# Kernel optimization log

Measured on AMD Instinct MI355X. Metric: run time of the kernel, lower is better.

## Reference

```python
import jax, jax.numpy as jnp
import numpy as np

H = 16        # num_attention_heads
KV = 4        # num_key_value_heads
HD = 128      # head_dim = hidden // H
N_REP = H // KV
ROPE_THETA = 10000.0


def _rope_cos_sin(T, dtype):
    inv_freq = 1.0 / (ROPE_THETA ** (jnp.arange(0, HD, 2, dtype=jnp.float32) / HD))
    pos = jnp.arange(T, dtype=jnp.float32)
    freqs = pos[:, None] * inv_freq[None, :]            # [T, HD/2]
    emb = jnp.concatenate([freqs, freqs], axis=-1)      # [T, HD]
    return jnp.cos(emb).astype(dtype), jnp.sin(emb).astype(dtype)


def _rotate_half(t):
    t1, t2 = jnp.split(t, 2, axis=-1)
    return jnp.concatenate([-t2, t1], axis=-1)


def setup_inputs() -> dict:
    key = jax.random.key(0)
    k1, k2, k3 = jax.random.split(key, 3)
    B, T, C = 2, 2048, 2048
    x = jax.random.normal(k1, (B, T, C), dtype=jnp.float32)
    attention_mask = jnp.ones((B, T), dtype=jnp.float32)
    w_qkv = jax.random.normal(k2, ((H + 2 * KV) * HD, C), dtype=jnp.float32) * 0.02
    w_proj = jax.random.normal(k3, (C, C), dtype=jnp.float32) * 0.02
    return {"x": x, "attention_mask": attention_mask, "w_qkv": w_qkv, "w_proj": w_proj}


def reference(x, attention_mask, w_qkv, w_proj):
    B, T, C = x.shape
    dtype = x.dtype
    neg = jnp.finfo(dtype).min

    # additive mask: causal (-big above diagonal) + padding ((1-mask)*min)
    i = jnp.arange(T)
    causal = jnp.where(i[None, :] <= i[:, None], 0.0, neg).astype(dtype)  # [T,T]
    add_mask = (1.0 - attention_mask)[:, None, None, :] * neg + causal[None, None]  # [B,1,T,T]

    # fused QKV projection
    qkv = jnp.einsum('btc,oc->bto', x, w_qkv)
    q = qkv[..., : H * HD].reshape(B, T, H, HD)
    k = qkv[..., H * HD : (H + KV) * HD].reshape(B, T, KV, HD)
    v = qkv[..., (H + KV) * HD :].reshape(B, T, KV, HD)

    # RoPE on q and k
    cos, sin = _rope_cos_sin(T, dtype)
    cos = cos[None, :, None, :]
    sin = sin[None, :, None, :]
    q = q * cos + _rotate_half(q) * sin
    k = k * cos + _rotate_half(k) * sin

    # GQA: repeat_interleave KV heads
    k = jnp.repeat(k, N_REP, axis=2)  # [B,T,H,HD]
    v = jnp.repeat(v, N_REP, axis=2)

    # [B,H,T,HD]
    q, k, v = (jnp.transpose(t, (0, 2, 1, 3)) for t in (q, k, v))

    scores = jnp.einsum('bhqd,bhkd->bhqk', q, k) * (1.0 / np.sqrt(HD))
    att = jax.nn.softmax(scores + add_mask, axis=-1)
    y = jnp.einsum('bhqk,bhkd->bhqd', att, v)
    y = jnp.transpose(y, (0, 2, 1, 3)).reshape(B, T, C)
    return jnp.einsum('btc,oc->bto', y, w_proj)
```

## Files before the change

kernel.cpp:

```cpp
#include <hip/hip_runtime.h>
#include <hip/hip_bf16.h>
#include <stdint.h>

typedef unsigned short u16;
typedef __attribute__((ext_vector_type(4))) float f32x4;
typedef __attribute__((ext_vector_type(8))) __bf16 bf16x8;
typedef __attribute__((ext_vector_type(8))) unsigned short u16x8;

#define NB 2
#define NT 2048
#define NC 2048
#define NH 16
#define NKV 4
#define HD 128
#define NQKV 3072
#define NQT 32
#define SCALE2 0.12751739f

__device__ __forceinline__ u16 f2bf(float f) {
  union { float f; uint32_t u; } c; c.f = f;
  uint32_t u = c.u + 0x7fffu + ((c.u >> 16) & 1u);
  return (u16)(u >> 16);
}
__device__ __forceinline__ float bf2f(u16 h) {
  union { uint32_t u; float f; } c; c.u = ((uint32_t)h) << 16;
  return c.f;
}
__device__ __forceinline__ uint32_t packbf2(float a, float b) {
  return (uint32_t)f2bf(a) | ((uint32_t)f2bf(b) << 16);
}

__device__ __forceinline__ void gload16(const void* g, void* lds) {
  __builtin_amdgcn_global_load_lds(
      (__attribute__((address_space(1))) void*)(uintptr_t)g,
      (__attribute__((address_space(3))) void*)(uint32_t)(uintptr_t)lds,
      16, 0, 0);
}

__global__ void cvt_bf16_kernel(const float* __restrict__ in, u16* __restrict__ out, int n4) {
  int i = blockIdx.x * blockDim.x + threadIdx.x;
  if (i >= n4) return;
  float4 v = ((const float4*)in)[i];
  uint32_t lo = (uint32_t)f2bf(v.x) | ((uint32_t)f2bf(v.y) << 16);
  uint32_t hi = (uint32_t)f2bf(v.z) | ((uint32_t)f2bf(v.w) << 16);
  ((uint2*)out)[i] = make_uint2(lo, hi);
}

__global__ void rope_tab_kernel(float* __restrict__ tab) {
  int idx = blockIdx.x * blockDim.x + threadIdx.x;
  int t = idx >> 6, i = idx & 63;
  float inv = expf(-(float)(2 * i) * (9.210340371976184f / 128.f));
  float f = (float)t * inv;
  tab[t * 128 + i] = cosf(f);
  tab[t * 128 + 64 + i] = sinf(f);
}

__global__ void rope_apply_kernel(const u16* __restrict__ qkv, const float* __restrict__ tab,
                                  u16* __restrict__ Q, u16* __restrict__ K) {
  int idx = blockIdx.x * blockDim.x + threadIdx.x;
  int i = idx & 63;
  int rest = idx >> 6;
  int hh = rest % 20;
  int bt = rest / 20;
  int t = bt & (NT - 1);
  int b = bt >> 11;
  const u16* src_row = qkv + (long)bt * NQKV;
  float c = tab[t * 128 + i], s = tab[t * 128 + 64 + i];
  if (hh < NH) {
    const u16* sp = src_row + hh * HD;
    float x0 = bf2f(sp[i]), x1 = bf2f(sp[i + 64]);
    u16* dp = Q + ((long)(b * NH + hh) * NT + t) * HD;
    dp[i] = f2bf((x0 * c - x1 * s) * SCALE2);
    dp[i + 64] = f2bf((x1 * c + x0 * s) * SCALE2);
  } else {
    int kh = hh - NH;
    const u16* sp = src_row + (NH + kh) * HD;
    float x0 = bf2f(sp[i]), x1 = bf2f(sp[i + 64]);
    u16* dp = K + ((long)(b * NKV + kh) * NT + t) * HD;
    dp[i] = f2bf(x0 * c - x1 * s);
    dp[i + 64] = f2bf(x1 * c + x0 * s);
  }
}

__global__ void vtrans_kernel(const u16* __restrict__ qkv, u16* __restrict__ Vt) {
  __shared__ u16 tile[64][72];
  const int t0 = (blockIdx.x >> 1) * 64;
  const int d0 = (blockIdx.x & 1) * 64;
  const int bkh = blockIdx.y;
  const int tid = threadIdx.x;
  const int tr = tid >> 2;
  const int tc = (tid & 3) * 16;
  const u16* src = qkv + ((long)((bkh >> 2) * NT) + t0 + tr) * NQKV +
                   (NH + NKV) * HD + (bkh & 3) * HD + d0 + tc;
  uint4 v0 = *(const uint4*)(src);
  uint4 v1 = *(const uint4*)(src + 8);
  *(uint4*)&tile[tr][tc] = v0;
  *(uint4*)&tile[tr][tc + 8] = v1;
  __syncthreads();
  const int dr = tid >> 2;
  const int tcc = (tid & 3) * 16;
  uint32_t pk[8];
#pragma unroll
  for (int e = 0; e < 8; ++e) {
    u16 a = tile[tcc + 2 * e][dr];
    u16 bq = tile[tcc + 2 * e + 1][dr];
    pk[e] = (uint32_t)a | ((uint32_t)bq << 16);
  }
  u16* dst = Vt + ((long)bkh * HD + d0 + dr) * NT + t0 + tcc;
  *(uint4*)(dst) = *(uint4*)&pk[0];
  *(uint4*)(dst + 8) = *(uint4*)&pk[4];
}

template <int OUT_BF16>
__global__ __launch_bounds__(256) void gemm_bt_kernel(const u16* __restrict__ A,
                                                      const u16* __restrict__ Bm,
                                                      void* __restrict__ Cm,
                                                      int M, int N, int K) {
  __shared__ __align__(16) u16 As[128 * 32];
  __shared__ __align__(16) u16 Bs[128 * 32];
  const int tid = threadIdx.x;
  const int lane = tid & 63;
  const int wid = tid >> 6;
  const long row0 = (long)blockIdx.y * 128;
  const long col0 = (long)blockIdx.x * 128;
  const int wr = (wid >> 1) * 64;
  const int wc = (wid & 1) * 64;
  const int g = lane >> 4;
  const int r = lane & 15;
  const int crow = lane >> 2;
  const int ccol = (lane & 3) * 8;
  const int c0 = wid * 2, c1 = wid * 2 + 1;

  f32x4 acc[4][4] = {};

  const u16* Abase0 = A + (row0 + c0 * 16 + crow) * (long)K + ccol;
  const u16* Abase1 = A + (row0 + c1 * 16 + crow) * (long)K + ccol;
  const u16* Bbase0 = Bm + (col0 + c0 * 16 + crow) * (long)K + ccol;
  const u16* Bbase1 = Bm + (col0 + c1 * 16 + crow) * (long)K + ccol;

  for (int k0 = 0; k0 < K; k0 += 32) {
    gload16(Abase0 + k0, &As[c0 * 512]);
    gload16(Abase1 + k0, &As[c1 * 512]);
    gload16(Bbase0 + k0, &Bs[c0 * 512]);
    gload16(Bbase1 + k0, &Bs[c1 * 512]);
    __syncthreads();
    bf16x8 af[4], bfr[4];
#pragma unroll
    for (int mi = 0; mi < 4; ++mi)
      af[mi] = *(const bf16x8*)&As[(wr + mi * 16 + r) * 32 + 8 * g];
#pragma unroll
    for (int ni = 0; ni < 4; ++ni)
      bfr[ni] = *(const bf16x8*)&Bs[(wc + ni * 16 + r) * 32 + 8 * g];
#pragma unroll
    for (int mi = 0; mi < 4; ++mi)
#pragma unroll
      for (int ni = 0; ni < 4; ++ni)
        acc[mi][ni] = __builtin_amdgcn_mfma_f32_16x16x32_bf16(af[mi], bfr[ni], acc[mi][ni], 0, 0, 0);
    __syncthreads();
  }
#pragma unroll
  for (int mi = 0; mi < 4; ++mi)
#pragma unroll
    for (int ni = 0; ni < 4; ++ni)
#pragma unroll
      for (int j = 0; j < 4; ++j) {
        long rr = row0 + wr + mi * 16 + g * 4 + j;
        long cc = col0 + wc + ni * 16 + r;
        float v = acc[mi][ni][j];
        if (OUT_BF16) ((u16*)Cm)[rr * N + cc] = f2bf(v);
        else          ((float*)Cm)[rr * N + cc] = v;
      }
}

__global__ __launch_bounds__(256) void attn_kernel(const u16* __restrict__ Qg,
                                                   const u16* __restrict__ Kg,
                                                   const u16* __restrict__ Vtg,
                                                   const float* __restrict__ amask,
                                                   u16* __restrict__ Y) {
  __shared__ __align__(16) u16 Ks[2][64 * 128];
  __shared__ __align__(16) u16 Vt[2][128 * 64];
  __shared__ __align__(16) u16 Ps[4][16 * 72];
  const int tid = threadIdx.x, lane = tid & 63, wid = tid >> 6;
  const int g = lane >> 4, r = lane & 15;
  const int h = blockIdx.y, b = blockIdx.z;
  const int kh = h >> 2;
  const int qta = blockIdx.x, qtb = NQT - 1 - qta;

  const u16* Kbh = Kg + (long)(b * NKV + kh) * NT * HD;
  const u16* Vtbh = Vtg + (long)(b * NKV + kh) * HD * NT;
  const u16* Qbh = Qg + (long)(b * NH + h) * NT * HD;
  const float* am_b = amask + b * NT;
  u16* Pw = &Ps[wid][0];

  const int total = qta + 1 + qtb + 1;

  const int krow_l = lane >> 4;
  const int kchunk = lane & 15;
  auto stageK = [&](u16* dst, int kv0) {
#pragma unroll
    for (int ii = 0; ii < 4; ++ii) {
      int kvl = (wid * 4 + ii) * 4 + krow_l;
      const u16* src = Kbh + (long)(kv0 + kvl) * HD + ((kchunk ^ (kvl & 7)) * 8);
      gload16(src, dst + (wid * 4 + ii) * 512);
    }
  };
  const int vrow_l = lane >> 3;
  const int vchunk = lane & 7;
  auto stageVt = [&](u16* dst, int kv0) {
#pragma unroll
    for (int ii = 0; ii < 4; ++ii) {
      int d = (wid * 4 + ii) * 8 + vrow_l;
      const u16* src = Vtbh + (long)d * NT + kv0 + ((vchunk ^ (d & 7)) * 8);
      gload16(src, dst + (wid * 4 + ii) * 512);
    }
  };

  bf16x8 qf[4];
  auto loadQ = [&](int q0) {
    const u16* Qrow = Qbh + (long)(q0 + wid * 16 + r) * HD;
#pragma unroll
    for (int kc = 0; kc < 4; ++kc)
      qf[kc] = *(const bf16x8*)(Qrow + kc * 32 + 8 * g);
  };

  stageK(Ks[0], 0);
  stageVt(Vt[0], 0);
  loadQ(qta * 64);
  __syncthreads();

  float m = -INFINITY;
  f32x4 lacc = {};
  f32x4 o[8] = {};
  int buf = 0;

  for (int i = 0; i < total; ++i) {
    const bool passA = (i <= qta);
    const int q0 = (passA ? qta : qtb) * 64;
    const int kt = passA ? i : i - qta - 1;
    const int kv0 = kt * 64;
    const bool diag = (i == qta) || (i == total - 1);
    const int qi = q0 + wid * 16 + r;

    if (i + 1 < total) {
      const int ktn = (i + 1 <= qta) ? i + 1 : i - qta;
      stageK(Ks[buf ^ 1], ktn * 64);
      stageVt(Vt[buf ^ 1], ktn * 64);
    }

    const u16* Ksb = Ks[buf];
    const u16* Vtb = Vt[buf];

    f32x4 s[4];
    __builtin_amdgcn_s_setprio(1);
#pragma unroll
    for (int cb = 0; cb < 4; ++cb) {
      f32x4 acc = {};
      int row = cb * 16 + r;
      int swz = (r & 7) << 4;
#pragma unroll
      for (int kc = 0; kc < 4; ++kc) {
        bf16x8 kf = *(const bf16x8*)((const char*)Ksb + ((row * 256 + (kc * 32 + 8 * g) * 2) ^ swz));
        acc = __builtin_amdgcn_mfma_f32_16x16x32_bf16(kf, qf[kc], acc, 0, 0, 0);
      }
      s[cb] = acc;
    }
    __builtin_amdgcn_s_setprio(0);

    if (diag) {
#pragma unroll
      for (int cb = 0; cb < 4; ++cb)
#pragma unroll
        for (int jj = 0; jj < 4; ++jj) {
          int kvi = kv0 + cb * 16 + 4 * g + jj;
          if (kvi > qi) s[cb][jj] = -INFINITY;
        }
    }

    float mxl = s[0][0];
#pragma unroll
    for (int cb = 0; cb < 4; ++cb)
#pragma unroll
      for (int jj = 0; jj < 4; ++jj) mxl = fmaxf(mxl, s[cb][jj]);
    if (!__all(mxl <= m + 8.f)) {
      float mx = mxl;
      mx = fmaxf(mx, __shfl_xor(mx, 16));
      mx = fmaxf(mx, __shfl_xor(mx, 32));
      float mnew = fmaxf(m, mx);
      float alpha = exp2f(m - mnew);
      m = mnew;
      lacc[0] *= alpha; lacc[1] *= alpha; lacc[2] *= alpha; lacc[3] *= alpha;
#pragma unroll
      for (int nb = 0; nb < 8; ++nb) {
        o[nb][0] *= alpha; o[nb][1] *= alpha; o[nb][2] *= alpha; o[nb][3] *= alpha;
      }
    }

    float4 amv[4];
#pragma unroll
    for (int cb = 0; cb < 4; ++cb)
      amv[cb] = *(const float4*)(am_b + kv0 + cb * 16 + 4 * g);

    float p[4][4];
#pragma unroll
    for (int cb = 0; cb < 4; ++cb)
#pragma unroll
      for (int jj = 0; jj < 4; ++jj) {
        float pv = exp2f(s[cb][jj] - m) * (&amv[cb].x)[jj];
        p[cb][jj] = pv;
        lacc[jj] += pv;
      }

#pragma unroll
    for (int cb = 0; cb < 4; ++cb) {
      union { __bf16 hh[4]; uint2 u; } pk;
      pk.hh[0] = (__bf16)p[cb][0]; pk.hh[1] = (__bf16)p[cb][1];
      pk.hh[2] = (__bf16)p[cb][2]; pk.hh[3] = (__bf16)p[cb][3];
      *(uint2*)((char*)Pw + 144 * r + 32 * cb + 8 * g) = pk.u;
    }
    asm volatile("s_waitcnt lgkmcnt(0)" ::: "memory");
    __builtin_amdgcn_sched_barrier(0);

    __builtin_amdgcn_s_setprio(1);
#pragma unroll
    for (int kc = 0; kc < 2; ++kc) {
      bf16x8 pb = *(const bf16x8*)((const char*)Pw + 144 * r + kc * 64 + 16 * g);
#pragma unroll
      for (int nb = 0; nb < 8; ++nb) {
        int d = nb * 16 + r;
        bf16x8 va = *(const bf16x8*)((const char*)Vtb +
            ((d * 128 + (kc * 32 + 8 * g) * 2) ^ ((d & 7) << 4)));
        o[nb] = __builtin_amdgcn_mfma_f32_16x16x32_bf16(va, pb, o[nb], 0, 0, 0);
      }
    }
    __builtin_amdgcn_s_setprio(0);

    if (diag) {
      float l = (lacc[0] + lacc[1]) + (lacc[2] + lacc[3]);
      l += __shfl_xor(l, 16);
      l += __shfl_xor(l, 32);
      float invl = 1.f / l;
      u16* Yrow = Y + ((long)b * NT + qi) * NC + h * HD;
#pragma unroll
      for (int nb = 0; nb < 8; ++nb)
        *(uint2*)(Yrow + nb * 16 + 4 * g) =
            make_uint2(packbf2(o[nb][0] * invl, o[nb][1] * invl),
                       packbf2(o[nb][2] * invl, o[nb][3] * invl));
      if (i == qta) {
        m = -INFINITY;
        lacc = f32x4{};
#pragma unroll
        for (int nb = 0; nb < 8; ++nb) o[nb] = f32x4{};
        loadQ(qtb * 64);
      }
    }

    __syncthreads();
    buf ^= 1;
  }
}

extern "C" void kernel_launch(void* const* d_in, const int* in_sizes, int n_in,
                              void* d_out, int out_size, void* d_ws, size_t ws_size,
                              hipStream_t stream) {
  const float* x = (const float*)d_in[0];
  const float* amask = (const float*)d_in[1];
  const float* w_qkv = (const float*)d_in[2];
  const float* w_proj = (const float*)d_in[3];

  const long MT = (long)NB * NT;
  char* ws = (char*)d_ws;
  size_t off = 0;
  auto carve = [&](size_t bytes) -> char* {
    char* p = ws + off;
    off += (bytes + 255) & ~(size_t)255;
    return p;
  };
  u16* xb   = (u16*)carve((size_t)MT * NC * 2);
  u16* wqb  = (u16*)carve((size_t)NQKV * NC * 2);
  u16* wpb  = (u16*)carve((size_t)NC * NC * 2);
  u16* qkvb = (u16*)carve((size_t)MT * NQKV * 2);
  float* tab = (float*)carve((size_t)NT * 128 * 4);

  u16* Qb = xb;
  u16* Kb = wqb;
  u16* Vtb = wqb + (size_t)NB * NKV * NT * HD;
  u16* Yb = qkvb;

  {
    int n4 = (int)(MT * NC / 4);
    cvt_bf16_kernel<<<dim3((n4 + 255) / 256), dim3(256), 0, stream>>>(x, xb, n4);
    n4 = (int)((long)NQKV * NC / 4);
    cvt_bf16_kernel<<<dim3((n4 + 255) / 256), dim3(256), 0, stream>>>(w_qkv, wqb, n4);
    n4 = (int)((long)NC * NC / 4);
    cvt_bf16_kernel<<<dim3((n4 + 255) / 256), dim3(256), 0, stream>>>(w_proj, wpb, n4);
  }
  rope_tab_kernel<<<dim3(NT * 64 / 256), dim3(256), 0, stream>>>(tab);
  gemm_bt_kernel<1><<<dim3(NQKV / 128, MT / 128), dim3(256), 0, stream>>>(xb, wqb, qkvb, (int)MT, NQKV, NC);
  rope_apply_kernel<<<dim3(NB * NT * 20 * 64 / 256), dim3(256), 0, stream>>>(qkvb, tab, Qb, Kb);
  vtrans_kernel<<<dim3(NT / 64 * 2, NB * NKV), dim3(256), 0, stream>>>(qkvb, Vtb);
  attn_kernel<<<dim3(NQT / 2, NH, NB), dim3(256), 0, stream>>>(Qb, Kb, Vtb, amask, Yb);
  gemm_bt_kernel<0><<<dim3(NC / 128, MT / 128), dim3(256), 0, stream>>>(Yb, wpb, d_out, (int)MT, NC, NC);
}
```

Baseline: 236.7 us.

## Rework attention to 32x32x16 MFMA with register-resident P and tiled V layout

The attention kernel moves from 16x16x32 to 32x32x16 MFMA. Each wave now handles 32 query rows, so the query tile per block grows to 128 and the grid shrinks to 8x16x2. Probabilities stay in registers as the B operand, which removes the per-wave LDS round trip and its waitcnt, and the V-transpose kernel writes a tiled, pair-interleaved layout that matches the new LDS swizzle. The tradeoff is fewer blocks (256 with launch bounds of one block per SM), higher register pressure, and a layout change that must stay consistent between the two kernels.

```diff
diff --git a/kernel.cpp b/kernel.cpp
--- a/kernel.cpp
+++ b/kernel.cpp
@@ -4,8 +4,8 @@
 
 typedef unsigned short u16;
 typedef __attribute__((ext_vector_type(4))) float f32x4;
+typedef __attribute__((ext_vector_type(16))) float f32x16;
 typedef __attribute__((ext_vector_type(8))) __bf16 bf16x8;
-typedef __attribute__((ext_vector_type(8))) unsigned short u16x8;
 
 #define NB 2
 #define NT 2048
@@ -14,7 +14,6 @@
 #define NKV 4
 #define HD 128
 #define NQKV 3072
-#define NQT 32
 #define SCALE2 0.12751739f
 
 __device__ __forceinline__ u16 f2bf(float f) {
@@ -106,7 +105,13 @@
     u16 bq = tile[tcc + 2 * e + 1][dr];
     pk[e] = (uint32_t)a | ((uint32_t)bq << 16);
   }
-  u16* dst = Vt + ((long)bkh * HD + d0 + dr) * NT + t0 + tcc;
+  uint32_t tmp;
+  tmp = pk[2]; pk[2] = pk[4]; pk[4] = tmp;
+  tmp = pk[3]; pk[3] = pk[5]; pk[5] = tmp;
+  const int d = d0 + dr;
+  const int t = t0 + tcc;
+  u16* dst = Vt + (long)bkh * HD * NT + (long)(d >> 1) * (2 * NT) +
+             (t >> 6) * 128 + (d & 1) * 64 + (t & 48);
   *(uint4*)(dst) = *(uint4*)&pk[0];
   *(uint4*)(dst + 8) = *(uint4*)&pk[4];
 }
@@ -172,185 +177,175 @@
       }
 }
 
-__global__ __launch_bounds__(256) void attn_kernel(const u16* __restrict__ Qg,
-                                                   const u16* __restrict__ Kg,
-                                                   const u16* __restrict__ Vtg,
-                                                   const float* __restrict__ amask,
-                                                   u16* __restrict__ Y) {
+__global__ __launch_bounds__(256, 1) void attn_kernel(const u16* __restrict__ Qg,
+                                                      const u16* __restrict__ Kg,
+                                                      const u16* __restrict__ Vtg,
+                                                      const float* __restrict__ amask,
+                                                      u16* __restrict__ Y) {
   __shared__ __align__(16) u16 Ks[2][64 * 128];
-  __shared__ __align__(16) u16 Vt[2][128 * 64];
-  __shared__ __align__(16) u16 Ps[4][16 * 72];
+  __shared__ __align__(16) u16 Vs[2][64 * 128];
   const int tid = threadIdx.x, lane = tid & 63, wid = tid >> 6;
-  const int g = lane >> 4, r = lane & 15;
+  const int ql = lane & 31, hi = lane >> 5;
   const int h = blockIdx.y, b = blockIdx.z;
   const int kh = h >> 2;
-  const int qta = blockIdx.x, qtb = NQT - 1 - qta;
+  const int qta = blockIdx.x, qtb = 15 - qta;
 
   const u16* Kbh = Kg + (long)(b * NKV + kh) * NT * HD;
   const u16* Vtbh = Vtg + (long)(b * NKV + kh) * HD * NT;
   const u16* Qbh = Qg + (long)(b * NH + h) * NT * HD;
   const float* am_b = amask + b * NT;
-  u16* Pw = &Ps[wid][0];
-
-  const int total = qta + 1 + qtb + 1;
-
-  const int krow_l = lane >> 4;
-  const int kchunk = lane & 15;
+
+  const int lenA = 2 * qta + 2;
+  const int total = lenA + 2 * qtb + 2;
+
+  const int srow = lane >> 4;
+  const int schunk = lane & 15;
   auto stageK = [&](u16* dst, int kv0) {
 #pragma unroll
     for (int ii = 0; ii < 4; ++ii) {
-      int kvl = (wid * 4 + ii) * 4 + krow_l;
-      const u16* src = Kbh + (long)(kv0 + kvl) * HD + ((kchunk ^ (kvl & 7)) * 8);
-      gload16(src, dst + (wid * 4 + ii) * 512);
+      int kvl = wid * 16 + ii * 4 + srow;
+      const u16* src = Kbh + (long)(kv0 + kvl) * HD + ((schunk ^ (kvl & 15)) * 8);
+      gload16(src, dst + (wid * 16 + ii * 4) * 128);
     }
   };
-  const int vrow_l = lane >> 3;
-  const int vchunk = lane & 7;
-  auto stageVt = [&](u16* dst, int kv0) {
+  auto stageV = [&](u16* dst, int kv0) {
+    const u16* vb = Vtbh + (kv0 >> 6) * 128;
 #pragma unroll
     for (int ii = 0; ii < 4; ++ii) {
-      int d = (wid * 4 + ii) * 8 + vrow_l;
-      const u16* src = Vtbh + (long)d * NT + kv0 + ((vchunk ^ (d & 7)) * 8);
-      gload16(src, dst + (wid * 4 + ii) * 512);
+      int R = wid * 16 + ii * 4 + srow;
+      const u16* src = vb + (long)R * (2 * NT) + ((schunk ^ (R & 15)) * 8);
+      gload16(src, dst + (wid * 16 + ii * 4) * 128);
     }
   };
 
-  bf16x8 qf[4];
+  bf16x8 qf[8];
   auto loadQ = [&](int q0) {
-    const u16* Qrow = Qbh + (long)(q0 + wid * 16 + r) * HD;
-#pragma unroll
-    for (int kc = 0; kc < 4; ++kc)
-      qf[kc] = *(const bf16x8*)(Qrow + kc * 32 + 8 * g);
+    const u16* Qrow = Qbh + (long)(q0 + wid * 32 + ql) * HD;
+#pragma unroll
+    for (int ks = 0; ks < 8; ++ks)
+      qf[ks] = *(const bf16x8*)(Qrow + ks * 16 + 8 * hi);
   };
 
   stageK(Ks[0], 0);
-  stageVt(Vt[0], 0);
-  loadQ(qta * 64);
+  stageV(Vs[0], 0);
+  loadQ(qta * 128);
   __syncthreads();
 
   float m = -INFINITY;
   f32x4 lacc = {};
-  f32x4 o[8] = {};
+  f32x16 o[4] = {};
   int buf = 0;
 
   for (int i = 0; i < total; ++i) {
-    const bool passA = (i <= qta);
-    const int q0 = (passA ? qta : qtb) * 64;
-    const int kt = passA ? i : i - qta - 1;
+    const bool passA = (i < lenA);
+    const int qt = passA ? qta : qtb;
+    const int q0 = qt * 128;
+    const int kt = passA ? i : i - lenA;
     const int kv0 = kt * 64;
-    const bool diag = (i == qta) || (i == total - 1);
-    const int qi = q0 + wid * 16 + r;
+    const bool lastp = (i == lenA - 1) || (i == total - 1);
+    const int qi = q0 + wid * 32 + ql;
 
     if (i + 1 < total) {
-      const int ktn = (i + 1 <= qta) ? i + 1 : i - qta;
+      const int ktn = (i + 1 < lenA) ? i + 1 : i + 1 - lenA;
       stageK(Ks[buf ^ 1], ktn * 64);
-      stageVt(Vt[buf ^ 1], ktn * 64);
-    }
-
-    const u16* Ksb = Ks[buf];
-    const u16* Vtb = Vt[buf];
-
-    f32x4 s[4];
+      stageV(Vs[buf ^ 1], ktn * 64);
+    }
+
+    const char* Ksb = (const char*)Ks[buf];
+    const char* Vsb = (const char*)Vs[buf];
+
+    f32x16 s0 = {}, s1 = {};
     __builtin_amdgcn_s_setprio(1);
 #pragma unroll
-    for (int cb = 0; cb < 4; ++cb) {
-      f32x4 acc = {};
-      int row = cb * 16 + r;
-      int swz = (r & 7) << 4;
-#pragma unroll
-      for (int kc = 0; kc < 4; ++kc) {
-        bf16x8 kf = *(const bf16x8*)((const char*)Ksb + ((row * 256 + (kc * 32 + 8 * g) * 2) ^ swz));
-        acc = __builtin_amdgcn_mfma_f32_16x16x32_bf16(kf, qf[kc], acc, 0, 0, 0);
+    for (int ks = 0; ks < 8; ++ks) {
+      bf16x8 kf0 = *(const bf16x8*)(Ksb + ql * 256 + (((2 * ks + hi) ^ (ql & 15)) * 16));
+      bf16x8 kf1 = *(const bf16x8*)(Ksb + (32 + ql) * 256 + (((2 * ks + hi) ^ (ql & 15)) * 16));
+      s0 = __builtin_amdgcn_mfma_f32_32x32x16_bf16(kf0, qf[ks], s0, 0, 0, 0);
+      s1 = __builtin_amdgcn_mfma_f32_32x32x16_bf16(kf1, qf[ks], s1, 0, 0, 0);
+    }
+    __builtin_amdgcn_s_setprio(0);
+
+    if (kt >= 2 * qt) {
+#pragma unroll
+      for (int reg = 0; reg < 16; ++reg) {
+        int kvl = (reg & 3) + 8 * (reg >> 2) + 4 * hi;
+        if (kv0 + kvl > qi) s0[reg] = -INFINITY;
+        if (kv0 + 32 + kvl > qi) s1[reg] = -INFINITY;
       }
-      s[cb] = acc;
-    }
-    __builtin_amdgcn_s_setprio(0);
-
-    if (diag) {
-#pragma unroll
-      for (int cb = 0; cb < 4; ++cb)
-#pragma unroll
-        for (int jj = 0; jj < 4; ++jj) {
-          int kvi = kv0 + cb * 16 + 4 * g + jj;
-          if (kvi > qi) s[cb][jj] = -INFINITY;
-        }
-    }
-
-    float mxl = s[0][0];
-#pragma unroll
-    for (int cb = 0; cb < 4; ++cb)
-#pragma unroll
-      for (int jj = 0; jj < 4; ++jj) mxl = fmaxf(mxl, s[cb][jj]);
+    }
+
+    float mxl = s0[0];
+#pragma unroll
+    for (int reg = 0; reg < 16; ++reg) { mxl = fmaxf(mxl, s0[reg]); mxl = fmaxf(mxl, s1[reg]); }
     if (!__all(mxl <= m + 8.f)) {
-      float mx = mxl;
-      mx = fmaxf(mx, __shfl_xor(mx, 16));
-      mx = fmaxf(mx, __shfl_xor(mx, 32));
+      float mx = fmaxf(mxl, __shfl_xor(mxl, 32));
       float mnew = fmaxf(m, mx);
       float alpha = exp2f(m - mnew);
       m = mnew;
-      lacc[0] *= alpha; lacc[1] *= alpha; lacc[2] *= alpha; lacc[3] *= alpha;
-#pragma unroll
-      for (int nb = 0; nb < 8; ++nb) {
-        o[nb][0] *= alpha; o[nb][1] *= alpha; o[nb][2] *= alpha; o[nb][3] *= alpha;
+      lacc *= alpha;
+#pragma unroll
+      for (int dblk = 0; dblk < 4; ++dblk) o[dblk] *= alpha;
+    }
+
+    float4 am0[4], am1[4];
+#pragma unroll
+    for (int u = 0; u < 4; ++u) {
+      am0[u] = *(const float4*)(am_b + kv0 + 8 * u + 4 * hi);
+      am1[u] = *(const float4*)(am_b + kv0 + 32 + 8 * u + 4 * hi);
+    }
+#pragma unroll
+    for (int reg = 0; reg < 16; ++reg) {
+      float p0 = exp2f(s0[reg] - m) * (&am0[reg >> 2].x)[reg & 3];
+      float p1 = exp2f(s1[reg] - m) * (&am1[reg >> 2].x)[reg & 3];
+      s0[reg] = p0; s1[reg] = p1;
+      lacc[reg & 3] += p0 + p1;
+    }
+
+    bf16x8 pb[4];
+#pragma unroll
+    for (int ks = 0; ks < 4; ++ks) {
+      union { __bf16 hh[8]; bf16x8 v; } pk;
+      const int base = 8 * (ks & 1);
+#pragma unroll
+      for (int j = 0; j < 8; ++j)
+        pk.hh[j] = (__bf16)((ks >= 2) ? s1[base + j] : s0[base + j]);
+      pb[ks] = pk.v;
+    }
+
+    __builtin_amdgcn_s_setprio(1);
+#pragma unroll
+    for (int ks = 0; ks < 4; ++ks) {
+#pragma unroll
+      for (int dblk = 0; dblk < 4; ++dblk) {
+        int drow = dblk * 16 + (ql >> 1);
+        int gr = ((ql & 1) * 8 + 2 * ks + hi) ^ (drow & 15);
+        bf16x8 va = *(const bf16x8*)(Vsb + drow * 256 + gr * 16);
+        o[dblk] = __builtin_amdgcn_mfma_f32_32x32x16_bf16(va, pb[ks], o[dblk], 0, 0, 0);
       }
     }
-
-    float4 amv[4];
-#pragma unroll
-    for (int cb = 0; cb < 4; ++cb)
-      amv[cb] = *(const float4*)(am_b + kv0 + cb * 16 + 4 * g);
-
-    float p[4][4];
-#pragma unroll
-    for (int cb = 0; cb < 4; ++cb)
-#pragma unroll
-      for (int jj = 0; jj < 4; ++jj) {
-        float pv = exp2f(s[cb][jj] - m) * (&amv[cb].x)[jj];
-        p[cb][jj] = pv;
-        lacc[jj] += pv;
-      }
-
-#pragma unroll
-    for (int cb = 0; cb < 4; ++cb) {
-      union { __bf16 hh[4]; uint2 u; } pk;
-      pk.hh[0] = (__bf16)p[cb][0]; pk.hh[1] = (__bf16)p[cb][1];
-      pk.hh[2] = (__bf16)p[cb][2]; pk.hh[3] = (__bf16)p[cb][3];
-      *(uint2*)((char*)Pw + 144 * r + 32 * cb + 8 * g) = pk.u;
-    }
-    asm volatile("s_waitcnt lgkmcnt(0)" ::: "memory");
-    __builtin_amdgcn_sched_barrier(0);
-
-    __builtin_amdgcn_s_setprio(1);
-#pragma unroll
-    for (int kc = 0; kc < 2; ++kc) {
-      bf16x8 pb = *(const bf16x8*)((const char*)Pw + 144 * r + kc * 64 + 16 * g);
-#pragma unroll
-      for (int nb = 0; nb < 8; ++nb) {
-        int d = nb * 16 + r;
-        bf16x8 va = *(const bf16x8*)((const char*)Vtb +
-            ((d * 128 + (kc * 32 + 8 * g) * 2) ^ ((d & 7) << 4)));
-        o[nb] = __builtin_amdgcn_mfma_f32_16x16x32_bf16(va, pb, o[nb], 0, 0, 0);
-      }
-    }
     __builtin_amdgcn_s_setprio(0);
 
-    if (diag) {
+    if (lastp) {
       float l = (lacc[0] + lacc[1]) + (lacc[2] + lacc[3]);
-      l += __shfl_xor(l, 16);
       l += __shfl_xor(l, 32);
       float invl = 1.f / l;
       u16* Yrow = Y + ((long)b * NT + qi) * NC + h * HD;
 #pragma unroll
-      for (int nb = 0; nb < 8; ++nb)
-        *(uint2*)(Yrow + nb * 16 + 4 * g) =
-            make_uint2(packbf2(o[nb][0] * invl, o[nb][1] * invl),
-                       packbf2(o[nb][2] * invl, o[nb][3] * invl));
-      if (i == qta) {
+      for (int dblk = 0; dblk < 4; ++dblk)
+#pragma unroll
+        for (int u = 0; u < 4; ++u) {
+          int d = dblk * 32 + 8 * u + 4 * hi;
+          int r0 = 4 * u;
+          *(uint2*)(Yrow + d) = make_uint2(
+              packbf2(o[dblk][r0] * invl, o[dblk][r0 + 1] * invl),
+              packbf2(o[dblk][r0 + 2] * invl, o[dblk][r0 + 3] * invl));
+        }
+      if (i != total - 1) {
         m = -INFINITY;
         lacc = f32x4{};
 #pragma unroll
-        for (int nb = 0; nb < 8; ++nb) o[nb] = f32x4{};
-        loadQ(qtb * 64);
+        for (int dblk = 0; dblk < 4; ++dblk) o[dblk] = f32x16{};
+        loadQ(qtb * 128);
       }
     }
 
@@ -398,6 +393,6 @@
   gemm_bt_kernel<1><<<dim3(NQKV / 128, MT / 128), dim3(256), 0, stream>>>(xb, wqb, qkvb, (int)MT, NQKV, NC);
   rope_apply_kernel<<<dim3(NB * NT * 20 * 64 / 256), dim3(256), 0, stream>>>(qkvb, tab, Qb, Kb);
   vtrans_kernel<<<dim3(NT / 64 * 2, NB * NKV), dim3(256), 0, stream>>>(qkvb, Vtb);
-  attn_kernel<<<dim3(NQT / 2, NH, NB), dim3(256), 0, stream>>>(Qb, Kb, Vtb, amask, Yb);
+  attn_kernel<<<dim3(8, NH, NB), dim3(256), 0, stream>>>(Qb, Kb, Vtb, amask, Yb);
   gemm_bt_kernel<0><<<dim3(NC / 128, MT / 128), dim3(256), 0, stream>>>(Yb, wpb, d_out, (int)MT, NC, NC);
 }
```

New measurement: 259.7 us. 1.1x slower.
